# Performance work log

Measured on AMD Instinct MI355X. Metric: run time of the kernel, lower is better.

The kernel has to match this reference:

```python
import jax, jax.numpy as jnp
from jax import lax
import numpy as np

FEAT_STRIDE = 16
PRE_NMS_TOP_N = 2000
POST_NMS_TOP_N = 300
NMS_THRESH = 0.7


def _whctrs(a):
    w = a[2] - a[0] + 1.0
    h = a[3] - a[1] + 1.0
    return w, h, a[0] + 0.5 * (w - 1.0), a[1] + 0.5 * (h - 1.0)


def _mkanchors(ws, hs, x_ctr, y_ctr):
    ws = np.asarray(ws, dtype=np.float64)
    hs = np.asarray(hs, dtype=np.float64)
    return np.stack([x_ctr - 0.5 * (ws - 1.0), y_ctr - 0.5 * (hs - 1.0),
                     x_ctr + 0.5 * (ws - 1.0), y_ctr + 0.5 * (hs - 1.0)], axis=1)


def generate_anchors(base_size=16, ratios=np.array([0.5, 1.0, 2.0]), scales=np.array([8.0, 16.0, 32.0])):
    base = np.array([1.0, 1.0, float(base_size), float(base_size)]) - 1.0
    w, h, xc, yc = _whctrs(base)
    size = w * h
    ws = np.round(np.sqrt(size / ratios))
    hs = np.round(ws * ratios)
    ratio_anchors = _mkanchors(ws, hs, xc, yc)
    out = []
    for i in range(ratio_anchors.shape[0]):
        w_i, h_i, xc_i, yc_i = _whctrs(ratio_anchors[i])
        out.append(_mkanchors(w_i * scales, h_i * scales, xc_i, yc_i))
    return np.vstack(out).astype(np.float32)


ANCHORS = generate_anchors()  # [A=9, 4]
NUM_ANCHORS = ANCHORS.shape[0]


def _nms_keep(boxes, thresh):
    # boxes [N,4], already sorted by descending score; torchvision IoU convention.
    x1, y1, x2, y2 = boxes[:, 0], boxes[:, 1], boxes[:, 2], boxes[:, 3]
    areas = (x2 - x1) * (y2 - y1)
    xx1 = jnp.maximum(x1[:, None], x1[None, :])
    yy1 = jnp.maximum(y1[:, None], y1[None, :])
    xx2 = jnp.minimum(x2[:, None], x2[None, :])
    yy2 = jnp.minimum(y2[:, None], y2[None, :])
    inter = jnp.clip(xx2 - xx1, 0.0) * jnp.clip(yy2 - yy1, 0.0)
    iou = inter / (areas[:, None] + areas[None, :] - inter + 1e-9)
    n = boxes.shape[0]
    # sup[i, j] True => box i (higher score) suppresses later box j
    sup = (iou > thresh) & jnp.triu(jnp.ones((n, n), bool), 1)

    def body(i, keep):
        return keep & ~(keep[i] & sup[i])

    return lax.fori_loop(0, n, body, jnp.ones((n,), bool))


def setup_inputs() -> dict:
    key = jax.random.key(0)
    k1, k2 = jax.random.split(key)
    B, A, H, W = 8, NUM_ANCHORS, 128, 128
    scores = jax.random.normal(k1, (B, 2 * A, H, W), jnp.float32)
    bbox_deltas = jax.random.normal(k2, (B, 4 * A, H, W), jnp.float32) * 0.2
    im_h = float(H * FEAT_STRIDE)
    im_w = float(W * FEAT_STRIDE)
    im_info = jnp.tile(jnp.array([[im_h, im_w, 1.0]], jnp.float32), (B, 1))
    return {"scores": scores, "bbox_deltas": bbox_deltas, "im_info": im_info}


def reference(scores, bbox_deltas, im_info):
    B, _, H, W = scores.shape
    A = NUM_ANCHORS
    # --- anchor generation over the feature grid ---
    sx = jnp.arange(W, dtype=jnp.float32) * FEAT_STRIDE
    sy = jnp.arange(H, dtype=jnp.float32) * FEAT_STRIDE
    gx, gy = jnp.meshgrid(sx, sy)  # 'xy' indexing matches np.meshgrid default
    shifts = jnp.stack([gx.ravel(), gy.ravel(), gx.ravel(), gy.ravel()], axis=1)  # [K,4]
    anchors = (jnp.asarray(ANCHORS)[None, :, :] + shifts[:, None, :]).reshape(-1, 4)  # [K*A,4]

    obj_scores = scores[:, A:].transpose(0, 2, 3, 1).reshape(B, -1)   # [B, K*A]
    deltas = bbox_deltas.transpose(0, 2, 3, 1).reshape(B, -1, 4)      # [B, K*A, 4]

    # --- bbox_transform_inv ---
    widths = anchors[:, 2] - anchors[:, 0] + 1.0
    heights = anchors[:, 3] - anchors[:, 1] + 1.0
    ctr_x = anchors[:, 0] + 0.5 * widths
    ctr_y = anchors[:, 1] + 0.5 * heights
    dx, dy, dw, dh = deltas[..., 0], deltas[..., 1], deltas[..., 2], deltas[..., 3]
    pred_ctr_x = dx * widths + ctr_x
    pred_ctr_y = dy * heights + ctr_y
    pred_w = jnp.exp(dw) * widths
    pred_h = jnp.exp(dh) * heights
    proposals = jnp.stack([pred_ctr_x - 0.5 * pred_w, pred_ctr_y - 0.5 * pred_h,
                           pred_ctr_x + 0.5 * pred_w, pred_ctr_y + 0.5 * pred_h], axis=-1)

    # --- clip_boxes: im_info[b] = (h, w, scale) ---
    max_x = (im_info[:, 1] - 1.0)[:, None]
    max_y = (im_info[:, 0] - 1.0)[:, None]
    proposals = jnp.stack([
        jnp.clip(proposals[..., 0], 0.0, max_x),
        jnp.clip(proposals[..., 1], 0.0, max_y),
        jnp.clip(proposals[..., 2], 0.0, max_x),
        jnp.clip(proposals[..., 3], 0.0, max_y)], axis=-1)

    # --- pre-NMS top-k by score ---
    _, order = lax.top_k(obj_scores, PRE_NMS_TOP_N)                  # [B, pre]
    top_props = jnp.take_along_axis(proposals, order[..., None], axis=1)  # [B, pre, 4]

    # --- per-image greedy NMS (fixed-size, jit-compatible) ---
    keep = jax.vmap(lambda b: _nms_keep(b, NMS_THRESH))(top_props)   # [B, pre] bool
    sel = jnp.argsort(jnp.where(keep, 0, 1), axis=1, stable=True)[:, :POST_NMS_TOP_N]
    valid = jnp.take_along_axis(keep, sel, axis=1)                   # [B, post]
    out_boxes = jnp.take_along_axis(top_props, sel[..., None], axis=1) * valid[..., None].astype(top_props.dtype)

    batch_idx = jnp.broadcast_to(
        jnp.arange(B, dtype=out_boxes.dtype)[:, None, None], (B, POST_NMS_TOP_N, 1))
    return jnp.concatenate([batch_idx, out_boxes], axis=-1)  # [B, post_nms_topN, 5]
```

## Files before the change

### kernel.cpp

```cpp
#include <hip/hip_runtime.h>

#define NB 8
#define NA 9
#define NCELL (128 * 128)
#define NTOT (NCELL * NA)
#define PRE_K 2000
#define POST_K 300
#define CAP2 8192
#define PARTS 18
#define NMS_TH 0.7f

__constant__ float c_aw[NA] = {184.f, 368.f, 736.f, 128.f, 256.f, 512.f, 88.f, 176.f, 352.f};
__constant__ float c_ah[NA] = {96.f, 192.f, 384.f, 128.f, 256.f, 512.f, 176.f, 352.f, 704.f};

__device__ __forceinline__ unsigned int sortable(float s) {
    unsigned int u = __float_as_uint(s);
    return (u & 0x80000000u) ? ~u : (u | 0x80000000u);
}

__device__ __forceinline__ unsigned long long shflx64(unsigned long long v, int m) {
    return __shfl_xor(v, m, 64);
}

__global__ __launch_bounds__(1024) void hist0_kernel(const float* __restrict__ scores,
                                                     unsigned int* __restrict__ h0out) {
    __shared__ unsigned int h[2048];
    int b = blockIdx.y, tid = threadIdx.x;
    h[tid] = 0; h[tid + 1024] = 0;
    __syncthreads();
    const float4* sp4 = (const float4*)(scores + (size_t)b * 18 * NCELL + (size_t)NA * NCELL);
    int base4 = blockIdx.x * 2048;
#pragma unroll
    for (int e = 0; e < 2; ++e) {
        float4 v = sp4[base4 + e * 1024 + tid];
        atomicAdd(&h[sortable(v.x) >> 21], 1u);
        atomicAdd(&h[sortable(v.y) >> 21], 1u);
        atomicAdd(&h[sortable(v.z) >> 21], 1u);
        atomicAdd(&h[sortable(v.w) >> 21], 1u);
    }
    __syncthreads();
    unsigned int* o = h0out + ((size_t)(b * PARTS + blockIdx.x)) * 2048;
    o[tid] = h[tid];
    o[tid + 1024] = h[tid + 1024];
}

__global__ __launch_bounds__(1024) void select0_kernel(const unsigned int* __restrict__ h0out,
                                                       uint2* __restrict__ state0,
                                                       unsigned int* __restrict__ gh1,
                                                       int* __restrict__ cnt) {
    __shared__ unsigned int wpart[16], wexcl[16];
    __shared__ unsigned int thr[1024];
    int b = blockIdx.x, tid = threadIdx.x;
    int lane = tid & 63, wid = tid >> 6;
    if (tid < 128) gh1[b * 128 + tid] = 0;
    if (tid == 0) cnt[b] = 0;
    unsigned int c0 = 0, c1 = 0;
    for (int p = 0; p < PARTS; ++p) {
        const unsigned int* hp = h0out + ((size_t)(b * PARTS + p)) * 2048;
        uint2 v = *(const uint2*)&hp[2 * tid];
        c0 += v.x; c1 += v.y;
    }
    unsigned int sum = c0 + c1;
#pragma unroll
    for (int off = 1; off < 64; off <<= 1) {
        unsigned int v = __shfl_down(sum, off, 64);
        if (lane + off < 64) sum += v;
    }
    if (lane == 0) wpart[wid] = sum;
    __syncthreads();
    if (tid < 16) {
        unsigned int e = 0;
        for (int w = tid + 1; w < 16; ++w) e += wpart[w];
        wexcl[tid] = e;
    }
    __syncthreads();
    unsigned int self = sum + wexcl[wid];
    thr[tid] = self;
    __syncthreads();
    unsigned int above = (tid < 1023) ? thr[tid + 1] : 0u;
    if (self >= (unsigned)PRE_K && above < (unsigned)PRE_K) {
        if (above + c1 >= (unsigned)PRE_K)
            state0[b] = make_uint2((unsigned)(2 * tid + 1), (unsigned)(PRE_K)-above);
        else
            state0[b] = make_uint2((unsigned)(2 * tid), (unsigned)(PRE_K)-above - c1);
    }
}

__global__ __launch_bounds__(1024) void gatherc_kernel(const float* __restrict__ scores,
                                                       const uint2* __restrict__ state0,
                                                       unsigned int* __restrict__ gh1,
                                                       int* __restrict__ cnt,
                                                       unsigned long long* __restrict__ buf) {
    __shared__ unsigned long long lbuf[2048];
    __shared__ unsigned int h128[128];
    __shared__ int lmisc[2];
    int b = blockIdx.y, tid = threadIdx.x;
    if (tid < 128) h128[tid] = 0;
    if (tid == 0) lmisc[0] = 0;
    __syncthreads();
    unsigned int piv = state0[b].x;
    unsigned int P = piv << 21;
    const float4* sp4 = (const float4*)(scores + (size_t)b * 18 * NCELL + (size_t)NA * NCELL);
    int base4 = blockIdx.x * 2048;
#pragma unroll
    for (int e = 0; e < 2; ++e) {
        int t4 = base4 + e * 1024 + tid;
        float4 v = sp4[t4];
        float el[4] = {v.x, v.y, v.z, v.w};
#pragma unroll
        for (int j = 0; j < 4; ++j) {
            unsigned int u = sortable(el[j]);
            if (u >= P) {
                if ((u >> 21) == piv) atomicAdd(&h128[(u >> 14) & 127u], 1u);
                int idx4 = t4 * 4 + j;
                int a = idx4 >> 14;
                int cell = idx4 & 16383;
                unsigned int i = (unsigned int)cell * 9u + (unsigned int)a;
                int pos = atomicAdd(&lmisc[0], 1);
                if (pos < 2048)
                    lbuf[pos] = ((unsigned long long)u << 32) |
                                (unsigned long long)(0xFFFFFFFFu - i);
            }
        }
    }
    __syncthreads();
    if (tid < 128 && h128[tid]) atomicAdd(&gh1[b * 128 + tid], h128[tid]);
    if (tid == 0) lmisc[1] = atomicAdd(&cnt[b], min(lmisc[0], 2048));
    __syncthreads();
    int m = min(lmisc[0], 2048), gb = lmisc[1];
    for (int t = tid; t < m; t += 1024) {
        int g = gb + t;
        if (g < CAP2) buf[(size_t)b * CAP2 + g] = lbuf[t];
    }
}

#define SHFL_STEP(J)                                                          \
    {                                                                         \
        int d_ = (J) >> 1;                                                    \
        bool keepMax = (((tid & d_) == 0) == (((2u * (unsigned)tid) & k) == 0)); \
        unsigned long long pa = shflx64(va, d_);                              \
        unsigned long long pb = shflx64(vb, d_);                              \
        va = keepMax ? (va > pa ? va : pa) : (va < pa ? va : pa);             \
        vb = keepMax ? (vb > pb ? vb : pb) : (vb < pb ? vb : pb);             \
    }
#define LOCAL_STEP()                                                          \
    {                                                                         \
        bool desc = (((2u * (unsigned)tid) & k) == 0);                        \
        unsigned long long lo = va < vb ? va : vb;                            \
        unsigned long long hi = va < vb ? vb : va;                            \
        va = desc ? hi : lo; vb = desc ? lo : hi;                             \
    }

__global__ __launch_bounds__(1024) void sortdec_kernel(const unsigned long long* __restrict__ buf,
                                                       const int* __restrict__ cnt,
                                                       const uint2* __restrict__ state0,
                                                       const unsigned int* __restrict__ gh1,
                                                       const float* __restrict__ deltas,
                                                       const float* __restrict__ im_info,
                                                       float4* __restrict__ props) {
    __shared__ unsigned long long s[4096];
    __shared__ unsigned int spiv;
    __shared__ int fcnt;
    int b = blockIdx.x, tid = threadIdx.x;
    if (tid == 0) fcnt = 0;
    if (tid < 64) {
        int lane = tid;
        unsigned int c0 = gh1[b * 128 + 2 * lane];
        unsigned int c1 = gh1[b * 128 + 2 * lane + 1];
        unsigned int sum = c0 + c1;
#pragma unroll
        for (int off = 1; off < 64; off <<= 1) {
            unsigned int v = __shfl_down(sum, off, 64);
            if (lane + off < 64) sum += v;
        }
        unsigned int above = __shfl_down(sum, 1, 64);
        if (lane == 63) above = 0;
        unsigned int need0 = state0[b].y;
        if (sum >= need0 && above < need0) {
            unsigned int d = (above + c1 >= need0) ? (unsigned)(2 * lane + 1) : (unsigned)(2 * lane);
            spiv = ((state0[b].x << 7) | d) << 14;
        }
    }
    __syncthreads();
    unsigned int P = spiv;
    int n = min(cnt[b], CAP2);
    const unsigned long long* src = buf + (size_t)b * CAP2;
    for (int t = tid; t < n; t += 1024) {
        unsigned long long e = src[t];
        if ((unsigned int)(e >> 32) >= P) {
            int pos = atomicAdd(&fcnt, 1);
            if (pos < 4096) s[pos] = e;
        }
    }
    __syncthreads();
    int n2 = min(fcnt, 4096);
    int SZ = (n2 <= 2048) ? 2048 : 4096;
    for (int t = tid; t < SZ; t += 1024)
        if (t >= n2) s[t] = 0ULL;
    __syncthreads();
    if (SZ == 2048) {
        unsigned long long va = s[2 * tid], vb = s[2 * tid + 1];
#pragma unroll
        for (unsigned k = 2; k <= 128; k <<= 1) {
#pragma unroll
            for (unsigned j = k >> 1; j >= 2; j >>= 1) SHFL_STEP(j)
            LOCAL_STEP()
        }
        for (unsigned k = 256; k <= 2048; k <<= 1) {
            s[2 * tid] = va; s[2 * tid + 1] = vb;
            __syncthreads();
            for (unsigned j = k >> 1; j >= 128; j >>= 1) {
                for (int t = tid; t < 2048; t += 1024) {
                    int ixj = t ^ (int)j;
                    if (ixj > t) {
                        unsigned long long x = s[t], y = s[ixj];
                        if ((((unsigned)t & k) == 0) ? (x < y) : (x > y)) { s[t] = y; s[ixj] = x; }
                    }
                }
                __syncthreads();
            }
            va = s[2 * tid]; vb = s[2 * tid + 1];
#pragma unroll
            for (unsigned j = 64; j >= 2; j >>= 1) SHFL_STEP(j)
            LOCAL_STEP()
        }
        s[2 * tid] = va; s[2 * tid + 1] = vb;
        __syncthreads();
    } else {
        for (int k = 2; k <= 4096; k <<= 1) {
            for (int j = k >> 1; j > 0; j >>= 1) {
                for (int t = tid; t < 4096; t += 1024) {
                    int ixj = t ^ j;
                    if (ixj > t) {
                        unsigned long long x = s[t], y = s[ixj];
                        if (((t & k) == 0) ? (x < y) : (x > y)) { s[t] = y; s[ixj] = x; }
                    }
                }
                __syncthreads();
            }
        }
    }
    float maxx = __fsub_rn(im_info[b * 3 + 1], 1.0f);
    float maxy = __fsub_rn(im_info[b * 3 + 0], 1.0f);
    const float* dbase = deltas + (size_t)b * 36 * NCELL;
    for (int r = tid; r < PRE_K; r += 1024) {
        unsigned int i = 0xFFFFFFFFu - (unsigned int)(s[r] & 0xFFFFFFFFu);
        unsigned int cell = i / 9u;
        unsigned int a = i - cell * 9u;
        int wx = (int)(cell & 127u), hy = (int)(cell >> 7);
        const float* dp = dbase + (size_t)(4u * a) * NCELL + (size_t)hy * 128 + wx;
        float dx = dp[0];
        float dy = dp[NCELL];
        float dw = dp[2 * NCELL];
        float dh = dp[3 * NCELL];
        float W_ = c_aw[a], H_ = c_ah[a];
        float cx = (float)(16 * wx + 8), cy = (float)(16 * hy + 8);
        float px = __fadd_rn(__fmul_rn(dx, W_), cx);
        float py = __fadd_rn(__fmul_rn(dy, H_), cy);
        float pw = __fmul_rn((float)exp((double)dw), W_);
        float ph = __fmul_rn((float)exp((double)dh), H_);
        float hw = __fmul_rn(0.5f, pw), hh = __fmul_rn(0.5f, ph);
        float x1 = __fsub_rn(px, hw), y1 = __fsub_rn(py, hh);
        float x2 = __fadd_rn(px, hw), y2 = __fadd_rn(py, hh);
        x1 = fminf(fmaxf(x1, 0.0f), maxx);
        y1 = fminf(fmaxf(y1, 0.0f), maxy);
        x2 = fminf(fmaxf(x2, 0.0f), maxx);
        y2 = fminf(fmaxf(y2, 0.0f), maxy);
        props[(size_t)b * PRE_K + r] = make_float4(x1, y1, x2, y2);
    }
}

__global__ void mask_kernel(const float4* __restrict__ boxes,
                            unsigned long long* __restrict__ colm) {
    int iT = blockIdx.x, jT = blockIdx.y, b = blockIdx.z;
    if (iT > jT) return;
    __shared__ float4 ib[64];
    int t = threadIdx.x;
    int i0 = iT * 64;
    ib[t] = (i0 + t < PRE_K) ? boxes[(size_t)b * PRE_K + i0 + t] : make_float4(0.f, 0.f, -1.f, -1.f);
    __syncthreads();
    int j = jT * 64 + t;
    if (j >= PRE_K) return;
    float4 jb = boxes[(size_t)b * PRE_K + j];
    float barea = __fmul_rn(__fsub_rn(jb.z, jb.x), __fsub_rn(jb.w, jb.y));
    unsigned long long m = 0ULL;
    for (int ii = 0; ii < 64; ++ii) {
        int i = i0 + ii;
        if (i < j) {
            float4 c = ib[ii];
            float aarea = __fmul_rn(__fsub_rn(c.z, c.x), __fsub_rn(c.w, c.y));
            float xx1 = fmaxf(c.x, jb.x), yy1 = fmaxf(c.y, jb.y);
            float xx2 = fminf(c.z, jb.z), yy2 = fminf(c.w, jb.w);
            float iw = fmaxf(__fsub_rn(xx2, xx1), 0.0f);
            float ih = fmaxf(__fsub_rn(yy2, yy1), 0.0f);
            float inter = __fmul_rn(iw, ih);
            float denom = __fadd_rn(__fsub_rn(__fadd_rn(aarea, barea), inter), 1e-9f);
            float iou = __fdiv_rn(inter, denom);
            if (iou > NMS_TH) m |= (1ULL << ii);
        }
    }
    colm[((size_t)b * 32 + iT) * 2048 + j] = m;
}

__global__ void scan_kernel(const unsigned long long* __restrict__ colm,
                            const float4* __restrict__ boxes,
                            float* __restrict__ out) {
    int b = blockIdx.x;
    int lane = threadIdx.x;
    __shared__ unsigned long long kw[32];
    __shared__ int keeplist[POST_K];
    const unsigned long long* cb = colm + (size_t)b * 32 * 2048;
    int total = 0;
    bool done = false;
    for (int k = 0; k < 32 && !done; ++k) {
        int j = k * 64 + lane;
        unsigned long long d = 0;
        int w = 0;
        for (; w + 4 <= k; w += 4) {
            unsigned long long a0 = cb[(size_t)(w + 0) * 2048 + j] & kw[w + 0];
            unsigned long long a1 = cb[(size_t)(w + 1) * 2048 + j] & kw[w + 1];
            unsigned long long a2 = cb[(size_t)(w + 2) * 2048 + j] & kw[w + 2];
            unsigned long long a3 = cb[(size_t)(w + 3) * 2048 + j] & kw[w + 3];
            d |= (a0 | a1) | (a2 | a3);
        }
        for (; w < k; ++w) d |= cb[(size_t)w * 2048 + j] & kw[w];
        unsigned long long diag = cb[(size_t)k * 2048 + j];
        bool alive_me = (d == 0ULL) && (j < PRE_K);
        unsigned long long alive = __ballot(alive_me);
        unsigned long long keptw = 0ULL;
        while (alive) {
            int i = __builtin_ctzll(alive);
            keptw |= (1ULL << i);
            if (lane == 0 && total < POST_K) keeplist[total] = k * 64 + i;
            total++;
            if (total >= POST_K) { done = true; break; }
            unsigned long long sup = __ballot(((diag >> i) & 1ULL) != 0ULL);
            alive &= ~sup;
            alive &= ~keptw;
        }
        if (lane == 0) kw[k] = keptw;
        __syncthreads();
    }
    __syncthreads();
    int K = min(total, POST_K);
    const float4* bb = boxes + (size_t)b * PRE_K;
    for (int r = lane; r < POST_K; r += 64) {
        float4 v = make_float4(0.f, 0.f, 0.f, 0.f);
        if (r < K) v = bb[keeplist[r]];
        float* o = out + ((size_t)b * POST_K + r) * 5;
        o[0] = (float)b;
        o[1] = v.x;
        o[2] = v.y;
        o[3] = v.z;
        o[4] = v.w;
    }
}

extern "C" void kernel_launch(void* const* d_in, const int* in_sizes, int n_in,
                              void* d_out, int out_size, void* d_ws, size_t ws_size,
                              hipStream_t stream) {
    const float* scores = (const float*)d_in[0];
    const float* deltas = (const float*)d_in[1];
    const float* im_info = (const float*)d_in[2];
    float* out = (float*)d_out;
    char* ws = (char*)d_ws;

    unsigned int* h0out = (unsigned int*)(ws + 0);
    unsigned int* gh1 = (unsigned int*)(ws + 1179648);
    uint2* state0 = (uint2*)(ws + 1183744);
    int* cnt = (int*)(ws + 1183808);
    unsigned long long* buf = (unsigned long long*)(ws + 1183872);
    float4* props = (float4*)(ws + 1708160);
    unsigned long long* colm = (unsigned long long*)(ws + 1966080);

    hipLaunchKernelGGL(hist0_kernel, dim3(PARTS, NB), dim3(1024), 0, stream, scores, h0out);
    hipLaunchKernelGGL(select0_kernel, dim3(NB), dim3(1024), 0, stream, h0out, state0, gh1, cnt);
    hipLaunchKernelGGL(gatherc_kernel, dim3(PARTS, NB), dim3(1024), 0, stream,
                       scores, state0, gh1, cnt, buf);
    hipLaunchKernelGGL(sortdec_kernel, dim3(NB), dim3(1024), 0, stream,
                       buf, cnt, state0, gh1, deltas, im_info, props);
    hipLaunchKernelGGL(mask_kernel, dim3(32, 32, NB), dim3(64), 0, stream, props, colm);
    hipLaunchKernelGGL(scan_kernel, dim3(NB), dim3(64), 0, stream, colm, props, out);
}
```

Measured before the change: 103.3 us.

## Fuse histogram and candidate gather into one sweep using a fixed threshold bin

Merges the histogram, pivot-select and gather kernels into a single sweep over the scores. The sweep builds the coarse histogram and at the same time buffers every element above a fixed threshold bin into per-block slots. The sort kernel now does the pivot selection itself and refines the pivot from the buffered candidates, falling back to a full rescan if a slot overflowed or the pivot lies below the threshold. This removes two launches and a second full pass over the scores. The fixed threshold is tuned to the score distribution, and the scan loop's unroll factor also goes from 4 to 8.

```diff
diff --git a/kernel.cpp b/kernel.cpp
--- a/kernel.cpp
+++ b/kernel.cpp
@@ -6,8 +6,9 @@
 #define NTOT (NCELL * NA)
 #define PRE_K 2000
 #define POST_K 300
-#define CAP2 8192
 #define PARTS 18
+#define SLOT 512
+#define THR_BIN 0x5FFu
 #define NMS_TH 0.7f
 
 __constant__ float c_aw[NA] = {184.f, 368.f, 736.f, 128.f, 256.f, 512.f, 88.f, 176.f, 352.f};
@@ -22,86 +23,19 @@
     return __shfl_xor(v, m, 64);
 }
 
-__global__ __launch_bounds__(1024) void hist0_kernel(const float* __restrict__ scores,
-                                                     unsigned int* __restrict__ h0out) {
+__global__ __launch_bounds__(1024) void sweep_kernel(const float* __restrict__ scores,
+                                                     unsigned int* __restrict__ h0out,
+                                                     int* __restrict__ bcnt,
+                                                     unsigned long long* __restrict__ buf) {
     __shared__ unsigned int h[2048];
-    int b = blockIdx.y, tid = threadIdx.x;
+    __shared__ unsigned long long lbuf[SLOT];
+    __shared__ int lcnt;
+    int b = blockIdx.y, part = blockIdx.x, tid = threadIdx.x;
     h[tid] = 0; h[tid + 1024] = 0;
+    if (tid == 0) lcnt = 0;
     __syncthreads();
     const float4* sp4 = (const float4*)(scores + (size_t)b * 18 * NCELL + (size_t)NA * NCELL);
-    int base4 = blockIdx.x * 2048;
-#pragma unroll
-    for (int e = 0; e < 2; ++e) {
-        float4 v = sp4[base4 + e * 1024 + tid];
-        atomicAdd(&h[sortable(v.x) >> 21], 1u);
-        atomicAdd(&h[sortable(v.y) >> 21], 1u);
-        atomicAdd(&h[sortable(v.z) >> 21], 1u);
-        atomicAdd(&h[sortable(v.w) >> 21], 1u);
-    }
-    __syncthreads();
-    unsigned int* o = h0out + ((size_t)(b * PARTS + blockIdx.x)) * 2048;
-    o[tid] = h[tid];
-    o[tid + 1024] = h[tid + 1024];
-}
-
-__global__ __launch_bounds__(1024) void select0_kernel(const unsigned int* __restrict__ h0out,
-                                                       uint2* __restrict__ state0,
-                                                       unsigned int* __restrict__ gh1,
-                                                       int* __restrict__ cnt) {
-    __shared__ unsigned int wpart[16], wexcl[16];
-    __shared__ unsigned int thr[1024];
-    int b = blockIdx.x, tid = threadIdx.x;
-    int lane = tid & 63, wid = tid >> 6;
-    if (tid < 128) gh1[b * 128 + tid] = 0;
-    if (tid == 0) cnt[b] = 0;
-    unsigned int c0 = 0, c1 = 0;
-    for (int p = 0; p < PARTS; ++p) {
-        const unsigned int* hp = h0out + ((size_t)(b * PARTS + p)) * 2048;
-        uint2 v = *(const uint2*)&hp[2 * tid];
-        c0 += v.x; c1 += v.y;
-    }
-    unsigned int sum = c0 + c1;
-#pragma unroll
-    for (int off = 1; off < 64; off <<= 1) {
-        unsigned int v = __shfl_down(sum, off, 64);
-        if (lane + off < 64) sum += v;
-    }
-    if (lane == 0) wpart[wid] = sum;
-    __syncthreads();
-    if (tid < 16) {
-        unsigned int e = 0;
-        for (int w = tid + 1; w < 16; ++w) e += wpart[w];
-        wexcl[tid] = e;
-    }
-    __syncthreads();
-    unsigned int self = sum + wexcl[wid];
-    thr[tid] = self;
-    __syncthreads();
-    unsigned int above = (tid < 1023) ? thr[tid + 1] : 0u;
-    if (self >= (unsigned)PRE_K && above < (unsigned)PRE_K) {
-        if (above + c1 >= (unsigned)PRE_K)
-            state0[b] = make_uint2((unsigned)(2 * tid + 1), (unsigned)(PRE_K)-above);
-        else
-            state0[b] = make_uint2((unsigned)(2 * tid), (unsigned)(PRE_K)-above - c1);
-    }
-}
-
-__global__ __launch_bounds__(1024) void gatherc_kernel(const float* __restrict__ scores,
-                                                       const uint2* __restrict__ state0,
-                                                       unsigned int* __restrict__ gh1,
-                                                       int* __restrict__ cnt,
-                                                       unsigned long long* __restrict__ buf) {
-    __shared__ unsigned long long lbuf[2048];
-    __shared__ unsigned int h128[128];
-    __shared__ int lmisc[2];
-    int b = blockIdx.y, tid = threadIdx.x;
-    if (tid < 128) h128[tid] = 0;
-    if (tid == 0) lmisc[0] = 0;
-    __syncthreads();
-    unsigned int piv = state0[b].x;
-    unsigned int P = piv << 21;
-    const float4* sp4 = (const float4*)(scores + (size_t)b * 18 * NCELL + (size_t)NA * NCELL);
-    int base4 = blockIdx.x * 2048;
+    int base4 = part * 2048;
 #pragma unroll
     for (int e = 0; e < 2; ++e) {
         int t4 = base4 + e * 1024 + tid;
@@ -110,28 +44,27 @@
 #pragma unroll
         for (int j = 0; j < 4; ++j) {
             unsigned int u = sortable(el[j]);
-            if (u >= P) {
-                if ((u >> 21) == piv) atomicAdd(&h128[(u >> 14) & 127u], 1u);
+            atomicAdd(&h[u >> 21], 1u);
+            if ((u >> 21) >= THR_BIN) {
                 int idx4 = t4 * 4 + j;
                 int a = idx4 >> 14;
                 int cell = idx4 & 16383;
                 unsigned int i = (unsigned int)cell * 9u + (unsigned int)a;
-                int pos = atomicAdd(&lmisc[0], 1);
-                if (pos < 2048)
+                int pos = atomicAdd(&lcnt, 1);
+                if (pos < SLOT)
                     lbuf[pos] = ((unsigned long long)u << 32) |
                                 (unsigned long long)(0xFFFFFFFFu - i);
             }
         }
     }
     __syncthreads();
-    if (tid < 128 && h128[tid]) atomicAdd(&gh1[b * 128 + tid], h128[tid]);
-    if (tid == 0) lmisc[1] = atomicAdd(&cnt[b], min(lmisc[0], 2048));
-    __syncthreads();
-    int m = min(lmisc[0], 2048), gb = lmisc[1];
-    for (int t = tid; t < m; t += 1024) {
-        int g = gb + t;
-        if (g < CAP2) buf[(size_t)b * CAP2 + g] = lbuf[t];
-    }
+    unsigned int* o = h0out + ((size_t)(b * PARTS + part)) * 2048;
+    o[tid] = h[tid];
+    o[tid + 1024] = h[tid + 1024];
+    if (tid == 0) bcnt[b * PARTS + part] = lcnt;
+    int m = min(lcnt, SLOT);
+    for (int t = tid; t < m; t += 1024)
+        buf[((size_t)(b * PARTS + part)) * SLOT + t] = lbuf[t];
 }
 
 #define SHFL_STEP(J)                                                          \
@@ -151,45 +84,136 @@
         va = desc ? hi : lo; vb = desc ? lo : hi;                             \
     }
 
-__global__ __launch_bounds__(1024) void sortdec_kernel(const unsigned long long* __restrict__ buf,
-                                                       const int* __restrict__ cnt,
-                                                       const uint2* __restrict__ state0,
-                                                       const unsigned int* __restrict__ gh1,
+__global__ __launch_bounds__(1024) void sortdec_kernel(const float* __restrict__ scores,
+                                                       const unsigned int* __restrict__ h0out,
+                                                       const int* __restrict__ bcnt,
+                                                       const unsigned long long* __restrict__ buf,
                                                        const float* __restrict__ deltas,
                                                        const float* __restrict__ im_info,
                                                        float4* __restrict__ props) {
     __shared__ unsigned long long s[4096];
-    __shared__ unsigned int spiv;
-    __shared__ int fcnt;
+    __shared__ unsigned int wpart[16], wexcl[16];
+    __shared__ unsigned int h128[128];
+    __shared__ int sbc[PARTS];
+    __shared__ unsigned int sh_piv, sh_spiv;
+    __shared__ unsigned int sh_need;
+    __shared__ int sh_ok, fcnt;
     int b = blockIdx.x, tid = threadIdx.x;
-    if (tid == 0) fcnt = 0;
+    int lane = tid & 63, wid = tid >> 6;
+    unsigned int* thr = (unsigned int*)s;
+
+    if (tid < PARTS) sbc[tid] = bcnt[b * PARTS + tid];
+    if (tid == 0) { sh_ok = 1; fcnt = 0; }
+
+    unsigned int c0 = 0, c1 = 0;
+    for (int p = 0; p < PARTS; ++p) {
+        const unsigned int* hp = h0out + ((size_t)(b * PARTS + p)) * 2048;
+        uint2 v = *(const uint2*)&hp[2 * tid];
+        c0 += v.x; c1 += v.y;
+    }
+    unsigned int sum = c0 + c1;
+#pragma unroll
+    for (int off = 1; off < 64; off <<= 1) {
+        unsigned int v = __shfl_down(sum, off, 64);
+        if (lane + off < 64) sum += v;
+    }
+    if (lane == 0) wpart[wid] = sum;
+    __syncthreads();
+    if (tid < 16) {
+        unsigned int e = 0;
+        for (int w = tid + 1; w < 16; ++w) e += wpart[w];
+        wexcl[tid] = e;
+    }
+    __syncthreads();
+    unsigned int self = sum + wexcl[wid];
+    thr[tid] = self;
+    __syncthreads();
+    unsigned int above = (tid < 1023) ? thr[tid + 1] : 0u;
+    if (self >= (unsigned)PRE_K && above < (unsigned)PRE_K) {
+        if (above + c1 >= (unsigned)PRE_K) {
+            sh_piv = (unsigned)(2 * tid + 1); sh_need = (unsigned)(PRE_K)-above;
+        } else {
+            sh_piv = (unsigned)(2 * tid); sh_need = (unsigned)(PRE_K)-above - c1;
+        }
+    }
+    __syncthreads();
+    unsigned int piv = sh_piv;
+    if (tid < PARTS && sbc[tid] > SLOT) sh_ok = 0;
+    if (tid == 0 && piv < THR_BIN) sh_ok = 0;
+    if (tid < 128) h128[tid] = 0;
+    __syncthreads();
+    int ok = sh_ok;
+
+    if (ok) {
+        for (int t = tid; t < PARTS * SLOT; t += 1024) {
+            int p = t >> 9, off = t & (SLOT - 1);
+            if (off < sbc[p]) {
+                unsigned long long e = buf[((size_t)(b * PARTS + p)) * SLOT + off];
+                unsigned int u = (unsigned int)(e >> 32);
+                if ((u >> 21) == piv) atomicAdd(&h128[(u >> 14) & 127u], 1u);
+            }
+        }
+    } else {
+        const float4* sp4 = (const float4*)(scores + (size_t)b * 18 * NCELL + (size_t)NA * NCELL);
+        for (int t = tid; t < NTOT / 4; t += 1024) {
+            float4 v = sp4[t];
+            unsigned int u;
+            u = sortable(v.x); if ((u >> 21) == piv) atomicAdd(&h128[(u >> 14) & 127u], 1u);
+            u = sortable(v.y); if ((u >> 21) == piv) atomicAdd(&h128[(u >> 14) & 127u], 1u);
+            u = sortable(v.z); if ((u >> 21) == piv) atomicAdd(&h128[(u >> 14) & 127u], 1u);
+            u = sortable(v.w); if ((u >> 21) == piv) atomicAdd(&h128[(u >> 14) & 127u], 1u);
+        }
+    }
+    __syncthreads();
     if (tid < 64) {
-        int lane = tid;
-        unsigned int c0 = gh1[b * 128 + 2 * lane];
-        unsigned int c1 = gh1[b * 128 + 2 * lane + 1];
-        unsigned int sum = c0 + c1;
+        unsigned int d0 = h128[2 * lane], d1 = h128[2 * lane + 1];
+        unsigned int rs = d0 + d1;
 #pragma unroll
         for (int off = 1; off < 64; off <<= 1) {
-            unsigned int v = __shfl_down(sum, off, 64);
-            if (lane + off < 64) sum += v;
-        }
-        unsigned int above = __shfl_down(sum, 1, 64);
-        if (lane == 63) above = 0;
-        unsigned int need0 = state0[b].y;
-        if (sum >= need0 && above < need0) {
-            unsigned int d = (above + c1 >= need0) ? (unsigned)(2 * lane + 1) : (unsigned)(2 * lane);
-            spiv = ((state0[b].x << 7) | d) << 14;
-        }
-    }
-    __syncthreads();
-    unsigned int P = spiv;
-    int n = min(cnt[b], CAP2);
-    const unsigned long long* src = buf + (size_t)b * CAP2;
-    for (int t = tid; t < n; t += 1024) {
-        unsigned long long e = src[t];
-        if ((unsigned int)(e >> 32) >= P) {
-            int pos = atomicAdd(&fcnt, 1);
-            if (pos < 4096) s[pos] = e;
+            unsigned int v = __shfl_down(rs, off, 64);
+            if (lane + off < 64) rs += v;
+        }
+        unsigned int rab = __shfl_down(rs, 1, 64);
+        if (lane == 63) rab = 0;
+        unsigned int need0 = sh_need;
+        if (rs >= need0 && rab < need0) {
+            unsigned int d = (rab + d1 >= need0) ? (unsigned)(2 * lane + 1) : (unsigned)(2 * lane);
+            sh_spiv = ((piv << 7) | d) << 14;
+        }
+    }
+    __syncthreads();
+    unsigned int spiv = sh_spiv;
+
+    if (ok) {
+        for (int t = tid; t < PARTS * SLOT; t += 1024) {
+            int p = t >> 9, off = t & (SLOT - 1);
+            if (off < sbc[p]) {
+                unsigned long long e = buf[((size_t)(b * PARTS + p)) * SLOT + off];
+                if ((unsigned int)(e >> 32) >= spiv) {
+                    int pos = atomicAdd(&fcnt, 1);
+                    if (pos < 4096) s[pos] = e;
+                }
+            }
+        }
+    } else {
+        const float4* sp4 = (const float4*)(scores + (size_t)b * 18 * NCELL + (size_t)NA * NCELL);
+        for (int t4 = tid; t4 < NTOT / 4; t4 += 1024) {
+            float4 v = sp4[t4];
+            float el[4] = {v.x, v.y, v.z, v.w};
+#pragma unroll
+            for (int j = 0; j < 4; ++j) {
+                unsigned int u = sortable(el[j]);
+                if (u >= spiv) {
+                    int idx4 = t4 * 4 + j;
+                    int a = idx4 >> 14;
+                    int cell = idx4 & 16383;
+                    unsigned int i = (unsigned int)cell * 9u + (unsigned int)a;
+                    int pos = atomicAdd(&fcnt, 1);
+                    if (pos < 4096)
+                        s[pos] = ((unsigned long long)u << 32) |
+                                 (unsigned long long)(0xFFFFFFFFu - i);
+                }
+            }
         }
     }
     __syncthreads();
@@ -198,6 +222,7 @@
     for (int t = tid; t < SZ; t += 1024)
         if (t >= n2) s[t] = 0ULL;
     __syncthreads();
+
     if (SZ == 2048) {
         unsigned long long va = s[2 * tid], vb = s[2 * tid + 1];
 #pragma unroll
@@ -240,6 +265,7 @@
             }
         }
     }
+
     float maxx = __fsub_rn(im_info[b * 3 + 1], 1.0f);
     float maxy = __fsub_rn(im_info[b * 3 + 0], 1.0f);
     const float* dbase = deltas + (size_t)b * 36 * NCELL;
@@ -316,12 +342,16 @@
         int j = k * 64 + lane;
         unsigned long long d = 0;
         int w = 0;
-        for (; w + 4 <= k; w += 4) {
+        for (; w + 8 <= k; w += 8) {
             unsigned long long a0 = cb[(size_t)(w + 0) * 2048 + j] & kw[w + 0];
             unsigned long long a1 = cb[(size_t)(w + 1) * 2048 + j] & kw[w + 1];
             unsigned long long a2 = cb[(size_t)(w + 2) * 2048 + j] & kw[w + 2];
             unsigned long long a3 = cb[(size_t)(w + 3) * 2048 + j] & kw[w + 3];
-            d |= (a0 | a1) | (a2 | a3);
+            unsigned long long a4 = cb[(size_t)(w + 4) * 2048 + j] & kw[w + 4];
+            unsigned long long a5 = cb[(size_t)(w + 5) * 2048 + j] & kw[w + 5];
+            unsigned long long a6 = cb[(size_t)(w + 6) * 2048 + j] & kw[w + 6];
+            unsigned long long a7 = cb[(size_t)(w + 7) * 2048 + j] & kw[w + 7];
+            d |= ((a0 | a1) | (a2 | a3)) | ((a4 | a5) | (a6 | a7));
         }
         for (; w < k; ++w) d |= cb[(size_t)w * 2048 + j] & kw[w];
         unsigned long long diag = cb[(size_t)k * 2048 + j];
@@ -366,19 +396,15 @@
     char* ws = (char*)d_ws;
 
     unsigned int* h0out = (unsigned int*)(ws + 0);
-    unsigned int* gh1 = (unsigned int*)(ws + 1179648);
-    uint2* state0 = (uint2*)(ws + 1183744);
-    int* cnt = (int*)(ws + 1183808);
-    unsigned long long* buf = (unsigned long long*)(ws + 1183872);
-    float4* props = (float4*)(ws + 1708160);
-    unsigned long long* colm = (unsigned long long*)(ws + 1966080);
-
-    hipLaunchKernelGGL(hist0_kernel, dim3(PARTS, NB), dim3(1024), 0, stream, scores, h0out);
-    hipLaunchKernelGGL(select0_kernel, dim3(NB), dim3(1024), 0, stream, h0out, state0, gh1, cnt);
-    hipLaunchKernelGGL(gatherc_kernel, dim3(PARTS, NB), dim3(1024), 0, stream,
-                       scores, state0, gh1, cnt, buf);
+    int* bcnt = (int*)(ws + 1179648);
+    unsigned long long* buf = (unsigned long long*)(ws + 1180672);
+    float4* props = (float4*)(ws + 1770496);
+    unsigned long long* colm = (unsigned long long*)(ws + 2026496);
+
+    hipLaunchKernelGGL(sweep_kernel, dim3(PARTS, NB), dim3(1024), 0, stream,
+                       scores, h0out, bcnt, buf);
     hipLaunchKernelGGL(sortdec_kernel, dim3(NB), dim3(1024), 0, stream,
-                       buf, cnt, state0, gh1, deltas, im_info, props);
+                       scores, h0out, bcnt, buf, deltas, im_info, props);
     hipLaunchKernelGGL(mask_kernel, dim3(32, 32, NB), dim3(64), 0, stream, props, colm);
     hipLaunchKernelGGL(scan_kernel, dim3(NB), dim3(64), 0, stream, colm, props, out);
 }
```

Result: no change. 102.3 us (-1.0%).
